# Kernel optimization log

Measured on AMD Instinct MI355X. Metric: run time of the kernel, lower is better.

## Reference

```python
import jax, jax.numpy as jnp
import numpy as np

B, P = 4, 2048
N = B * P
QD = 512            # query_dim == inner_dim (pos_emb is added to raw features)
CD = 512            # context_dim
HEADS, DH = 8, 64
INNER = HEADS * DH
SCALE = DH ** -0.5
HC, WC = 32, 32     # context spatial grid
L = HC * WC         # context_len
SELF_HW = 512       # spatial_dim[:2]
STRIDE = 8          # resolution_level == sparse tensor stride
PE_H = SELF_HW // STRIDE  # 64 BEV pos-emb grid


def setup_inputs() -> dict:
    key = jax.random.key(0)
    k = jax.random.split(key, 9)
    return {
        "feats": jax.random.normal(k[0], (N, QD), jnp.float32),
        "coords_xy": jax.random.randint(k[1], (N, 2), 0, SELF_HW),
        "context_emb": jax.random.normal(k[2], (B, HC, WC, CD), jnp.float32),
        "Wq": jax.random.normal(k[3], (QD, INNER), jnp.float32) * 0.02,
        "Wk": jax.random.normal(k[4], (CD, INNER), jnp.float32) * 0.02,
        "Wv": jax.random.normal(k[5], (CD, INNER), jnp.float32) * 0.02,
        "Wo": jax.random.normal(k[6], (INNER, QD), jnp.float32) * 0.02,
        "bo": jnp.zeros((QD,), jnp.float32),
        "pos_embedding": jax.random.normal(k[7], (PE_H, PE_H, INNER), jnp.float32) / INNER ** 0.5,
        "context_pos_embedding": jax.random.normal(k[8], (L, CD), jnp.float32) / INNER ** 0.5,
    }


def _neighbor_mask(coords_xy):
    # get_context_mask: scatter a (2*STRIDE+1)^2 neighborhood around each point's
    # projected context cell into a [N, L] boolean mask
    ratio = jnp.float32(HC) / jnp.float32(SELF_HW)
    center = jnp.round(coords_xy.astype(jnp.float32) * ratio).astype(jnp.int32)  # [N,2]
    off = jnp.stack(
        jnp.meshgrid(jnp.arange(-STRIDE, STRIDE + 1), jnp.arange(-STRIDE, STRIDE + 1), indexing="ij"),
        axis=-1,
    ).reshape(-1, 2)  # [K,2], K = 289
    pos = center[:, None, :] + off[None, :, :]        # [N,K,2]
    r = jnp.clip(pos[..., 0], 0, HC - 1)
    c = jnp.clip(pos[..., 1], 0, WC - 1)
    flat = r * WC + c                                  # [N,K]
    return jnp.zeros((N, L), jnp.bool_).at[jnp.arange(N)[:, None], flat].set(True)


def reference(feats, coords_xy, context_emb, Wq, Wk, Wv, Wo, bo, pos_embedding, context_pos_embedding):
    # get_context: add learned context positional embedding, flatten spatial -> [B, L, CD]
    ctx = (context_emb + context_pos_embedding.reshape(HC, WC, CD)).reshape(B, L, CD)
    # get_pos_emb: gather BEV positional embedding per point via floor(coord/stride)
    rc = coords_xy // STRIDE                           # [N,2] in [0, 64)
    pe = pos_embedding[rc[:, 0], rc[:, 1]]             # [N, INNER]
    f = (feats + pe).reshape(B, P, QD)                 # points grouped per batch (equal counts)
    mask = _neighbor_mask(coords_xy).reshape(B, P, L)
    q = (f @ Wq).reshape(B, P, HEADS, DH).transpose(0, 2, 1, 3)    # [B,h,P,d]
    k = (ctx @ Wk).reshape(B, L, HEADS, DH).transpose(0, 2, 1, 3)  # [B,h,L,d]
    v = (ctx @ Wv).reshape(B, L, HEADS, DH).transpose(0, 2, 1, 3)
    sim = jnp.einsum("bhid,bhjd->bhij", q, k) * SCALE              # [B,h,P,L]
    neg = -jnp.finfo(sim.dtype).max
    sim = jnp.where(mask[:, None, :, :], sim, neg)
    attn = jax.nn.softmax(sim, axis=-1)
    out = jnp.einsum("bhij,bhjd->bhid", attn, v)
    out = out.transpose(0, 2, 1, 3).reshape(B, P, INNER)
    out = out @ Wo + bo                                # to_out (dropout=0, eval)
    return out.reshape(N, QD)                          # scatter back to point features
```

## Files before the change

### kernel.cpp

```cpp
#include <hip/hip_runtime.h>


typedef __attribute__((ext_vector_type(8))) short bf16x8;
typedef __attribute__((ext_vector_type(4))) float f32x4;

#define SCL 0.18033688f

__device__ __forceinline__ unsigned short f2bf(float x) {
  union { float f; unsigned int u; } v; v.f = x;
  unsigned int r = v.u + 0x7FFFu + ((v.u >> 16) & 1u);
  return (unsigned short)(r >> 16);
}

__device__ __forceinline__ unsigned int pk2bf(float a, float b) {
  return (unsigned)f2bf(a) | ((unsigned)f2bf(b) << 16);
}

__device__ __forceinline__ unsigned int cvtpk(float a, float b) {
  unsigned int r;
  asm("v_cvt_pk_bf16_f32 %0, %1, %2" : "=v"(r) : "v"(a), "v"(b));
  return r;
}

__device__ __forceinline__ float fexp2(float x) {
#if __has_builtin(__builtin_amdgcn_exp2f)
  return __builtin_amdgcn_exp2f(x);
#else
  return exp2f(x);
#endif
}

__device__ __forceinline__ int swzb(int row, int chk) {
  return row * 128 + ((chk * 16) ^ ((row & 7) << 4));
}

__global__ __launch_bounds__(256) void prep_w(const float* __restrict__ Wq, const float* __restrict__ Wk,
                                              const float* __restrict__ Wv, const float* __restrict__ Wo,
                                              unsigned short* __restrict__ Wqt, unsigned short* __restrict__ Wkt,
                                              unsigned short* __restrict__ Wvt, unsigned short* __restrict__ Wot) {
  __shared__ float tile[64][65];
  const int bid = blockIdx.x;
  const int wsel = bid >> 6, tt = bid & 63;
  const int kt = (tt >> 3) << 6, ntb = (tt & 7) << 6;
  const float* W = (wsel == 0) ? Wq : (wsel == 1) ? Wk : (wsel == 2) ? Wv : Wo;
  unsigned short* Wt = (wsel == 0) ? Wqt : (wsel == 1) ? Wkt : (wsel == 2) ? Wvt : Wot;
  const int t = threadIdx.x;
#pragma unroll
  for (int p = 0; p < 16; ++p) {
    int e = p * 256 + t;
    int row = e >> 6, col = e & 63;
    tile[row][col] = W[(long)(kt + row) * 512 + ntb + col];
  }
  __syncthreads();
#pragma unroll
  for (int p = 0; p < 16; ++p) {
    int e = p * 256 + t;
    int n = e >> 6, k = e & 63;
    Wt[(long)(ntb + n) * 512 + kt + k] = f2bf(tile[k][n]);
  }
}

__global__ __launch_bounds__(256) void prep_in(const float* __restrict__ feats,
                                               const int* __restrict__ coords,
                                               const float* __restrict__ pos_emb,
                                               const float* __restrict__ ctx,
                                               const float* __restrict__ ctx_pos,
                                               unsigned short* __restrict__ Aq,
                                               unsigned short* __restrict__ Ac,
                                               int* __restrict__ perm) {
  if (blockIdx.x >= 6144) {
    __shared__ int hist[64];
    __shared__ int base[64];
    const int bb = blockIdx.x - 6144;
    const int t = threadIdx.x;
    if (t < 64) hist[t] = 0;
    __syncthreads();
    int keys[8];
#pragma unroll
    for (int i = 0; i < 8; ++i) {
      int q = bb * 2048 + t * 8 + i;
      int cr = (int)rintf((float)coords[2 * q] * 0.0625f);
      keys[i] = cr;
      atomicAdd(&hist[cr], 1);
    }
    __syncthreads();
    if (t == 0) {
      int s = 0;
      for (int k2 = 0; k2 < 64; ++k2) { base[k2] = s; s += hist[k2]; }
    }
    __syncthreads();
#pragma unroll
    for (int i = 0; i < 8; ++i) {
      int pos = atomicAdd(&base[keys[i]], 1);
      perm[bb * 2048 + pos] = t * 8 + i;
    }
    return;
  }
  int i = blockIdx.x * 256 + threadIdx.x;
  if (i < 1048576) {
    int e = i << 2;
    int q = e >> 9, k = e & 511;
    int pi = ((coords[2 * q] >> 3) << 6) + (coords[2 * q + 1] >> 3);
    float4 a = *(const float4*)(feats + e);
    float4 p = *(const float4*)(pos_emb + ((size_t)pi << 9) + k);
    uint2 o;
    o.x = pk2bf(a.x + p.x, a.y + p.y);
    o.y = pk2bf(a.z + p.z, a.w + p.w);
    *(uint2*)(Aq + e) = o;
  } else {
    int e = (i - 1048576) << 2;
    int r = e >> 9, k = e & 511;
    float4 a = *(const float4*)(ctx + e);
    float4 p = *(const float4*)(ctx_pos + ((size_t)(r & 1023) << 9) + k);
    uint2 o;
    o.x = pk2bf(a.x + p.x, a.y + p.y);
    o.y = pk2bf(a.z + p.z, a.w + p.w);
    *(uint2*)(Ac + e) = o;
  }
}

__global__ __launch_bounds__(256) void gemm_qkv(const unsigned short* __restrict__ Aq,
                                                const unsigned short* __restrict__ Ac,
                                                const unsigned short* __restrict__ Wqt,
                                                const unsigned short* __restrict__ Wkt,
                                                const unsigned short* __restrict__ Wvt,
                                                unsigned short* __restrict__ Qb,
                                                unsigned short* __restrict__ Kb,
                                                unsigned short* __restrict__ Vt) {
  __shared__ unsigned short As[128][72];
  __shared__ unsigned short Bs[128][72];
  const int t = threadIdx.x, l = t & 63, wid = t >> 6;
  const int wr = (wid >> 1) << 6, wc = (wid & 1) << 6;
  const int orig = blockIdx.x;
  const int bx = (orig & 7) * 64 + (orig >> 3);
  const bool isQ = bx < 256;
  long tm; const unsigned short* Bt; const unsigned short* Ab; bool isV = false; int nt;
  if (isQ) {
    tm = (long)(bx >> 2) * 128;
    nt = bx & 3;
    Bt = Wqt + (long)nt * 65536;
    Ab = Aq;
  } else {
    const int kvx = bx - 256;
    tm = (long)(kvx >> 3) * 128;
    const int y = kvx & 7;
    isV = y >= 4; nt = y & 3;
    Bt = (isV ? Wvt : Wkt) + (long)nt * 65536;
    Ab = Ac;
  }

  f32x4 acc[4][4] = {};
  const int lr = l & 15, lk = (l >> 4) << 3;
  const int srw = t >> 3, sch = (t & 7) << 3;

  for (int s = 0; s < 8; ++s) {
    const int k0 = s << 6;
    int4 rav[4], rbv[4];
#pragma unroll
    for (int p = 0; p < 4; ++p) {
      int row = srw + (p << 5);
      rav[p] = *(const int4*)(Ab + (tm + row) * 512 + k0 + sch);
      rbv[p] = *(const int4*)(Bt + (long)row * 512 + k0 + sch);
    }
#pragma unroll
    for (int p = 0; p < 4; ++p) {
      int row = srw + (p << 5);
      *(int4*)(&As[row][sch]) = rav[p];
      *(int4*)(&Bs[row][sch]) = rbv[p];
    }
    __syncthreads();
#pragma unroll
    for (int kk = 0; kk < 2; ++kk) {
      bf16x8 af[4], bfr[4];
#pragma unroll
      for (int i = 0; i < 4; ++i) af[i]  = *(const bf16x8*)(&As[wr + i * 16 + lr][kk * 32 + lk]);
#pragma unroll
      for (int i = 0; i < 4; ++i) bfr[i] = *(const bf16x8*)(&Bs[wc + i * 16 + lr][kk * 32 + lk]);
#pragma unroll
      for (int mi = 0; mi < 4; ++mi)
#pragma unroll
        for (int ni = 0; ni < 4; ++ni)
          acc[mi][ni] = __builtin_amdgcn_mfma_f32_16x16x32_bf16(af[mi], bfr[ni], acc[mi][ni], 0, 0, 0);
    }
    __syncthreads();
  }

  const int lq = (l >> 4) << 2;
#pragma unroll
  for (int mi = 0; mi < 4; ++mi)
#pragma unroll
    for (int ni = 0; ni < 4; ++ni) {
      int cn = nt * 128 + wc + ni * 16 + lr;
      long r0 = tm + wr + mi * 16 + lq;
      if (isQ) {
#pragma unroll
        for (int r = 0; r < 4; ++r)
          Qb[(r0 + r) * 512 + cn] = f2bf(acc[mi][ni][r] * SCL);
      } else if (!isV) {
#pragma unroll
        for (int r = 0; r < 4; ++r)
          Kb[(r0 + r) * 512 + cn] = f2bf(acc[mi][ni][r]);
      } else {
        int h = cn >> 6, d = cn & 63;
#pragma unroll
        for (int r = 0; r < 4; ++r) {
          long row = r0 + r;
          int b = (int)(row >> 10), j = (int)(row & 1023);
          int jp = (j & ~63) | ((j & 15) << 2) | ((j >> 4) & 3);
          Vt[((long)(b * 8 + h) * 64 + d) * 1024 + jp] = f2bf(acc[mi][ni][r]);
        }
      }
    }
}

__global__ __launch_bounds__(512, 4) void attn_mfma(const unsigned short* __restrict__ Qb,
                                                    const unsigned short* __restrict__ Kb,
                                                    const unsigned short* __restrict__ Vt,
                                                    const int* __restrict__ coords,
                                                    const int* __restrict__ perm,
                                                    unsigned short* __restrict__ Abf) {
  __shared__ char Kl[2][8192];
  __shared__ char Vl[2][8192];
  __shared__ char Ol[2048];
  __shared__ unsigned short Plds[8][16][72];
  __shared__ int permL[128];
  __shared__ int rng[2];
  const int t = threadIdx.x, w = t >> 6, l = t & 63;
  const int g = l >> 4, lc = l & 15;
  const int orig = blockIdx.x;
  const int sw = (orig & 7) * 64 + (orig >> 3);
  const int qx = sw & 15, bh = sw >> 4;
  const int b = bh >> 3, h = bh & 7;

  if (t < 128) permL[t] = perm[b * 2048 + qx * 128 + t];
  if (t == 0) { rng[0] = 63; rng[1] = 0; }
  __syncthreads();

  int rm[4], cm[4];
  int lrmin = 63, lrmax = 0;
#pragma unroll
  for (int r = 0; r < 4; ++r) {
    long qq = (long)b * 2048 + permL[w * 16 + g * 4 + r];
    int cr = (int)rintf((float)coords[2 * qq] * 0.0625f);
    int cc = (int)rintf((float)coords[2 * qq + 1] * 0.0625f);
    int rlo = max(0, cr - 8), rhi = min(31, cr + 8);
    int clo = max(0, cc - 8), chi = min(31, cc + 8);
    rm[r] = (int)((((unsigned)1 << (rhi - rlo + 1)) - 1) << rlo);
    cm[r] = (int)((((unsigned)1 << (chi - clo + 1)) - 1) << clo);
    lrmin = min(lrmin, rlo); lrmax = max(lrmax, rhi);
  }
#pragma unroll
  for (int off = 32; off > 0; off >>= 1) {
    lrmin = min(lrmin, __shfl_xor(lrmin, off));
    lrmax = max(lrmax, __shfl_xor(lrmax, off));
  }
  if (l == 0) { atomicMin(&rng[0], lrmin); atomicMax(&rng[1], lrmax); }

  bf16x8 qfr[2];
  {
    long qrow = (long)b * 2048 + permL[w * 16 + lc];
#pragma unroll
    for (int dc = 0; dc < 2; ++dc)
      qfr[dc] = *(const bf16x8*)(Qb + qrow * 512 + h * 64 + dc * 32 + g * 8);
  }

  const int srow = t >> 3, schk = t & 7;
  const unsigned short* Kg = Kb + ((long)b * 1024) * 512 + h * 64;
  const unsigned short* Vg = Vt + ((long)bh * 64) * 1024;

  if (t < 128) {
    int r = t >> 3, c = t & 7;
    unsigned short vv = (r == 0) ? (unsigned short)0x3F80 : (unsigned short)0;
    unsigned short tmp[8] = {vv, vv, vv, vv, vv, vv, vv, vv};
    *(int4*)(Ol + swzb(r, c)) = *(int4*)tmp;
  }
  __syncthreads();
  const int t0 = rng[0] >> 1, t1 = rng[1] >> 1;
  {
    const int kb0 = t0 * 64;
    int4 sk = *(const int4*)(Kg + (long)(kb0 + srow) * 512 + schk * 8);
    int4 sv_ = *(const int4*)(Vg + (long)srow * 1024 + kb0 + schk * 8);
    *(int4*)(Kl[0] + swzb(srow, schk)) = sk;
    *(int4*)(Vl[0] + swzb(srow, schk)) = sv_;
  }
  __syncthreads();

  f32x4 po[5] = {};

  for (int kt = t0; kt <= t1; ++kt) {
    const int cur = (kt - t0) & 1;
    const int kb = kt * 64;
    int4 nk = {}, nv = {};
    if (kt < t1) {
      const int kbn = kb + 64;
      nk = *(const int4*)(Kg + (long)(kbn + srow) * 512 + schk * 8);
      nv = *(const int4*)(Vg + (long)srow * 1024 + kbn + schk * 8);
    }

    bf16x8 kfr[4][2];
#pragma unroll
    for (int kf = 0; kf < 4; ++kf)
#pragma unroll
      for (int dc = 0; dc < 2; ++dc)
        kfr[kf][dc] = *(const bf16x8*)(Kl[cur] + swzb(kf * 16 + lc, dc * 4 + g));

    f32x4 sv[4];
#pragma unroll
    for (int kf = 0; kf < 4; ++kf) {
      f32x4 a = {};
      a = __builtin_amdgcn_mfma_f32_16x16x32_bf16(qfr[0], kfr[kf][0], a, 0, 0, 0);
      a = __builtin_amdgcn_mfma_f32_16x16x32_bf16(qfr[1], kfr[kf][1], a, 0, 0, 0);
      sv[kf] = a;
    }

    const int jrb = kb >> 5;
    int cmk[4][4];
#pragma unroll
    for (int kf = 0; kf < 4; ++kf) {
      int jr = jrb + (kf >> 1);
#pragma unroll
      for (int r = 0; r < 4; ++r)
        cmk[kf][r] = ((rm[r] >> jr) & 1) ? cm[r] : 0;
    }
#pragma unroll
    for (int kf = 0; kf < 4; ++kf) {
      int jc = ((kf & 1) << 4) + lc;
#pragma unroll
      for (int r = 0; r < 4; ++r) {
        float p = fexp2(sv[kf][r]);
        sv[kf][r] = ((cmk[kf][r] >> jc) & 1) ? p : 0.0f;
      }
    }

    bf16x8 vfr[5][2];
#pragma unroll
    for (int df = 0; df < 4; ++df)
#pragma unroll
      for (int kc = 0; kc < 2; ++kc)
        vfr[df][kc] = *(const bf16x8*)(Vl[cur] + swzb(df * 16 + lc, kc * 4 + g));
#pragma unroll
    for (int kc = 0; kc < 2; ++kc)
      vfr[4][kc] = *(const bf16x8*)(Ol + swzb(lc, kc * 4 + g));

#pragma unroll
    for (int r = 0; r < 4; ++r) {
      uint2 pk;
      pk.x = cvtpk(sv[0][r], sv[1][r]);
      pk.y = cvtpk(sv[2][r], sv[3][r]);
      *(uint2*)(&Plds[w][g * 4 + r][4 * lc]) = pk;
    }

    bf16x8 pa0 = *(const bf16x8*)(&Plds[w][lc][g * 8]);
    bf16x8 pa1 = *(const bf16x8*)(&Plds[w][lc][32 + g * 8]);
    __builtin_amdgcn_s_setprio(1);
#pragma unroll
    for (int df = 0; df < 5; ++df) {
      po[df] = __builtin_amdgcn_mfma_f32_16x16x32_bf16(pa0, vfr[df][0], po[df], 0, 0, 0);
      po[df] = __builtin_amdgcn_mfma_f32_16x16x32_bf16(pa1, vfr[df][1], po[df], 0, 0, 0);
    }
    __builtin_amdgcn_s_setprio(0);

    if (kt < t1) {
      const int nxt = cur ^ 1;
      *(int4*)(Kl[nxt] + swzb(srow, schk)) = nk;
      *(int4*)(Vl[nxt] + swzb(srow, schk)) = nv;
    }
    __syncthreads();
  }

#pragma unroll
  for (int r = 0; r < 4; ++r) {
    float lsum = __shfl(po[4][r], l & 48);
    float inv = 1.0f / lsum;
    long qr = (long)b * 2048 + permL[w * 16 + g * 4 + r];
#pragma unroll
    for (int df = 0; df < 4; ++df)
      Abf[qr * 512 + h * 64 + df * 16 + lc] = f2bf(po[df][r] * inv);
  }
}

__global__ __launch_bounds__(256) void gemm_o(const unsigned short* __restrict__ A,
                                              const unsigned short* __restrict__ Bt,
                                              float* __restrict__ C,
                                              const float* __restrict__ bias) {
  __shared__ unsigned short As[64][72];
  __shared__ unsigned short Bs[128][72];
  const int t = threadIdx.x, l = t & 63, wid = t >> 6;
  const int wr = (wid >> 1) << 5;
  const int wc = (wid & 1) << 6;
  const int orig = blockIdx.x;
  const int bx = (orig & 7) * 64 + (orig >> 3);
  const long tm = (long)(bx >> 2) * 64;
  const long tn = (long)(bx & 3) * 128;

  f32x4 acc[2][4] = {};
  const int lr = l & 15, lk = (l >> 4) << 3;
  for (int s = 0; s < 8; ++s) {
    const int k0 = s << 6;
    int4 rAv[2], rBv[4];
#pragma unroll
    for (int p = 0; p < 2; ++p) {
      int e = p * 256 + t;
      int row = e >> 3, ch = (e & 7) << 3;
      rAv[p] = *(const int4*)(A + (tm + row) * 512 + k0 + ch);
    }
#pragma unroll
    for (int p = 0; p < 4; ++p) {
      int e = p * 256 + t;
      int row = e >> 3, ch = (e & 7) << 3;
      rBv[p] = *(const int4*)(Bt + (tn + row) * 512 + k0 + ch);
    }
#pragma unroll
    for (int p = 0; p < 2; ++p) {
      int e = p * 256 + t;
      int row = e >> 3, ch = (e & 7) << 3;
      *(int4*)(&As[row][ch]) = rAv[p];
    }
#pragma unroll
    for (int p = 0; p < 4; ++p) {
      int e = p * 256 + t;
      int row = e >> 3, ch = (e & 7) << 3;
      *(int4*)(&Bs[row][ch]) = rBv[p];
    }
    __syncthreads();
#pragma unroll
    for (int kk = 0; kk < 2; ++kk) {
      bf16x8 af[2], bfr[4];
#pragma unroll
      for (int i = 0; i < 2; ++i) af[i]  = *(const bf16x8*)(&As[wr + i * 16 + lr][kk * 32 + lk]);
#pragma unroll
      for (int i = 0; i < 4; ++i) bfr[i] = *(const bf16x8*)(&Bs[wc + i * 16 + lr][kk * 32 + lk]);
#pragma unroll
      for (int mi = 0; mi < 2; ++mi)
#pragma unroll
        for (int ni = 0; ni < 4; ++ni)
          acc[mi][ni] = __builtin_amdgcn_mfma_f32_16x16x32_bf16(af[mi], bfr[ni], acc[mi][ni], 0, 0, 0);
    }
    __syncthreads();
  }

  const int lq = (l >> 4) << 2;
#pragma unroll
  for (int mi = 0; mi < 2; ++mi)
#pragma unroll
    for (int ni = 0; ni < 4; ++ni) {
      long col = tn + wc + ni * 16 + lr;
      float bv = bias[col];
      long r0 = tm + wr + mi * 16 + lq;
#pragma unroll
      for (int r = 0; r < 4; ++r)
        C[(r0 + r) * 512 + col] = acc[mi][ni][r] + bv;
    }
}

extern "C" void kernel_launch(void* const* d_in, const int* in_sizes, int n_in,
                              void* d_out, int out_size, void* d_ws, size_t ws_size,
                              hipStream_t stream) {
  (void)in_sizes; (void)n_in; (void)out_size; (void)ws_size;
  const float* feats   = (const float*)d_in[0];
  const int*   coords  = (const int*)d_in[1];
  const float* ctx     = (const float*)d_in[2];
  const float* Wq      = (const float*)d_in[3];
  const float* Wk      = (const float*)d_in[4];
  const float* Wv      = (const float*)d_in[5];
  const float* Wo      = (const float*)d_in[6];
  const float* bo      = (const float*)d_in[7];
  const float* pos_emb = (const float*)d_in[8];
  const float* ctx_pos = (const float*)d_in[9];
  float* out = (float*)d_out;
  char* ws = (char*)d_ws;

  unsigned short* Wqt = (unsigned short*)(ws);
  unsigned short* Wkt = (unsigned short*)(ws + 524288);
  unsigned short* Wvt = (unsigned short*)(ws + 1048576);
  unsigned short* Wot = (unsigned short*)(ws + 1572864);
  unsigned short* Aq  = (unsigned short*)(ws + 2097152);
  unsigned short* Ac  = (unsigned short*)(ws + 10485760);
  unsigned short* Qb  = (unsigned short*)(ws + 14680064);
  unsigned short* Kb  = (unsigned short*)(ws + 23068672);
  unsigned short* Vt  = (unsigned short*)(ws + 27262976);
  unsigned short* Abf = (unsigned short*)(ws + 31457280);
  int*            prm = (int*)(ws + 39845888);

  prep_w  <<<256, 256, 0, stream>>>(Wq, Wk, Wv, Wo, Wqt, Wkt, Wvt, Wot);
  prep_in <<<6148, 256, 0, stream>>>(feats, coords, pos_emb, ctx, ctx_pos, Aq, Ac, prm);
  gemm_qkv<<<512, 256, 0, stream>>>(Aq, Ac, Wqt, Wkt, Wvt, Qb, Kb, Vt);
  attn_mfma<<<512, 512, 0, stream>>>(Qb, Kb, Vt, coords, prm, Abf);
  gemm_o  <<<512, 256, 0, stream>>>(Abf, Wot, out, bo);
}
```

Baseline: 91.79 us.

## Double-buffer GEMM tiles via direct global-to-LDS loads; skip masked attention tiles per wave

```diff
diff --git a/kernel.cpp b/kernel.cpp
--- a/kernel.cpp
+++ b/kernel.cpp
@@ -28,6 +28,12 @@
 #else
   return exp2f(x);
 #endif
+}
+
+__device__ __forceinline__ void gload16(const unsigned short* g, char* l) {
+  __builtin_amdgcn_global_load_lds(
+      (const __attribute__((address_space(1))) unsigned int*)g,
+      (__attribute__((address_space(3))) unsigned int*)l, 16, 0, 0);
 }
 
 __device__ __forceinline__ int swzb(int row, int chk) {
@@ -127,10 +133,10 @@
                                                 unsigned short* __restrict__ Qb,
                                                 unsigned short* __restrict__ Kb,
                                                 unsigned short* __restrict__ Vt) {
-  __shared__ unsigned short As[128][72];
-  __shared__ unsigned short Bs[128][72];
-  const int t = threadIdx.x, l = t & 63, wid = t >> 6;
-  const int wr = (wid >> 1) << 6, wc = (wid & 1) << 6;
+  __shared__ char Asf[2][16384];
+  __shared__ char Bsf[2][16384];
+  const int t = threadIdx.x, l = t & 63, wv = t >> 6;
+  const int wr = (wv >> 1) << 6, wc = (wv & 1) << 6;
   const int orig = blockIdx.x;
   const int bx = (orig & 7) * 64 + (orig >> 3);
   const bool isQ = bx < 256;
@@ -149,33 +155,37 @@
     Ab = Ac;
   }
 
+  const int rr = l >> 3, chs = (l & 7) ^ rr;
+  auto STAGE = [&](int buf, int k0) {
+#pragma unroll
+    for (int i = 0; i < 4; ++i) {
+      int c = (wv << 2) + i;
+      int row = (c << 3) + rr;
+      gload16(Ab + (tm + row) * 512 + k0 + chs * 8, Asf[buf] + (c << 10));
+      gload16(Bt + (long)row * 512 + k0 + chs * 8, Bsf[buf] + (c << 10));
+    }
+  };
+
+  STAGE(0, 0);
+  __syncthreads();
+
   f32x4 acc[4][4] = {};
-  const int lr = l & 15, lk = (l >> 4) << 3;
-  const int srw = t >> 3, sch = (t & 7) << 3;
+  const int lr = l & 15, g = l >> 4;
 
   for (int s = 0; s < 8; ++s) {
-    const int k0 = s << 6;
-    int4 rav[4], rbv[4];
-#pragma unroll
-    for (int p = 0; p < 4; ++p) {
-      int row = srw + (p << 5);
-      rav[p] = *(const int4*)(Ab + (tm + row) * 512 + k0 + sch);
-      rbv[p] = *(const int4*)(Bt + (long)row * 512 + k0 + sch);
-    }
-#pragma unroll
-    for (int p = 0; p < 4; ++p) {
-      int row = srw + (p << 5);
-      *(int4*)(&As[row][sch]) = rav[p];
-      *(int4*)(&Bs[row][sch]) = rbv[p];
-    }
-    __syncthreads();
+    const int cur = s & 1;
+    if (s < 7) STAGE(cur ^ 1, (s + 1) << 6);
 #pragma unroll
     for (int kk = 0; kk < 2; ++kk) {
+      const int chd = (kk << 2) + g;
       bf16x8 af[4], bfr[4];
 #pragma unroll
-      for (int i = 0; i < 4; ++i) af[i]  = *(const bf16x8*)(&As[wr + i * 16 + lr][kk * 32 + lk]);
-#pragma unroll
-      for (int i = 0; i < 4; ++i) bfr[i] = *(const bf16x8*)(&Bs[wc + i * 16 + lr][kk * 32 + lk]);
+      for (int i = 0; i < 4; ++i) {
+        int ra = wr + i * 16 + lr;
+        int rb = wc + i * 16 + lr;
+        af[i]  = *(const bf16x8*)(Asf[cur] + swzb(ra, chd));
+        bfr[i] = *(const bf16x8*)(Bsf[cur] + swzb(rb, chd));
+      }
 #pragma unroll
       for (int mi = 0; mi < 4; ++mi)
 #pragma unroll
@@ -185,7 +195,7 @@
     __syncthreads();
   }
 
-  const int lq = (l >> 4) << 2;
+  const int lq = g << 2;
 #pragma unroll
   for (int mi = 0; mi < 4; ++mi)
 #pragma unroll
@@ -254,6 +264,7 @@
     lrmin = min(lrmin, __shfl_xor(lrmin, off));
     lrmax = max(lrmax, __shfl_xor(lrmax, off));
   }
+  const int wt0 = lrmin >> 1, wt1 = lrmax >> 1;
   if (l == 0) { atomicMin(&rng[0], lrmin); atomicMax(&rng[1], lrmax); }
 
   bf16x8 qfr[2];
@@ -297,68 +308,70 @@
       nv = *(const int4*)(Vg + (long)srow * 1024 + kbn + schk * 8);
     }
 
-    bf16x8 kfr[4][2];
-#pragma unroll
-    for (int kf = 0; kf < 4; ++kf)
-#pragma unroll
-      for (int dc = 0; dc < 2; ++dc)
-        kfr[kf][dc] = *(const bf16x8*)(Kl[cur] + swzb(kf * 16 + lc, dc * 4 + g));
-
-    f32x4 sv[4];
-#pragma unroll
-    for (int kf = 0; kf < 4; ++kf) {
-      f32x4 a = {};
-      a = __builtin_amdgcn_mfma_f32_16x16x32_bf16(qfr[0], kfr[kf][0], a, 0, 0, 0);
-      a = __builtin_amdgcn_mfma_f32_16x16x32_bf16(qfr[1], kfr[kf][1], a, 0, 0, 0);
-      sv[kf] = a;
-    }
-
-    const int jrb = kb >> 5;
-    int cmk[4][4];
-#pragma unroll
-    for (int kf = 0; kf < 4; ++kf) {
-      int jr = jrb + (kf >> 1);
-#pragma unroll
-      for (int r = 0; r < 4; ++r)
-        cmk[kf][r] = ((rm[r] >> jr) & 1) ? cm[r] : 0;
-    }
-#pragma unroll
-    for (int kf = 0; kf < 4; ++kf) {
-      int jc = ((kf & 1) << 4) + lc;
+    if (kt >= wt0 && kt <= wt1) {
+      bf16x8 kfr[4][2];
+#pragma unroll
+      for (int kf = 0; kf < 4; ++kf)
+#pragma unroll
+        for (int dc = 0; dc < 2; ++dc)
+          kfr[kf][dc] = *(const bf16x8*)(Kl[cur] + swzb(kf * 16 + lc, dc * 4 + g));
+
+      f32x4 sv[4];
+#pragma unroll
+      for (int kf = 0; kf < 4; ++kf) {
+        f32x4 a = {};
+        a = __builtin_amdgcn_mfma_f32_16x16x32_bf16(qfr[0], kfr[kf][0], a, 0, 0, 0);
+        a = __builtin_amdgcn_mfma_f32_16x16x32_bf16(qfr[1], kfr[kf][1], a, 0, 0, 0);
+        sv[kf] = a;
+      }
+
+      const int jrb = kb >> 5;
+      int cmk[4][4];
+#pragma unroll
+      for (int kf = 0; kf < 4; ++kf) {
+        int jr = jrb + (kf >> 1);
+#pragma unroll
+        for (int r = 0; r < 4; ++r)
+          cmk[kf][r] = ((rm[r] >> jr) & 1) ? cm[r] : 0;
+      }
+#pragma unroll
+      for (int kf = 0; kf < 4; ++kf) {
+        int jc = ((kf & 1) << 4) + lc;
+#pragma unroll
+        for (int r = 0; r < 4; ++r) {
+          float p = fexp2(sv[kf][r]);
+          sv[kf][r] = ((cmk[kf][r] >> jc) & 1) ? p : 0.0f;
+        }
+      }
+
+      bf16x8 vfr[5][2];
+#pragma unroll
+      for (int df = 0; df < 4; ++df)
+#pragma unroll
+        for (int kc = 0; kc < 2; ++kc)
+          vfr[df][kc] = *(const bf16x8*)(Vl[cur] + swzb(df * 16 + lc, kc * 4 + g));
+#pragma unroll
+      for (int kc = 0; kc < 2; ++kc)
+        vfr[4][kc] = *(const bf16x8*)(Ol + swzb(lc, kc * 4 + g));
+
 #pragma unroll
       for (int r = 0; r < 4; ++r) {
-        float p = fexp2(sv[kf][r]);
-        sv[kf][r] = ((cmk[kf][r] >> jc) & 1) ? p : 0.0f;
-      }
-    }
-
-    bf16x8 vfr[5][2];
-#pragma unroll
-    for (int df = 0; df < 4; ++df)
-#pragma unroll
-      for (int kc = 0; kc < 2; ++kc)
-        vfr[df][kc] = *(const bf16x8*)(Vl[cur] + swzb(df * 16 + lc, kc * 4 + g));
-#pragma unroll
-    for (int kc = 0; kc < 2; ++kc)
-      vfr[4][kc] = *(const bf16x8*)(Ol + swzb(lc, kc * 4 + g));
-
-#pragma unroll
-    for (int r = 0; r < 4; ++r) {
-      uint2 pk;
-      pk.x = cvtpk(sv[0][r], sv[1][r]);
-      pk.y = cvtpk(sv[2][r], sv[3][r]);
-      *(uint2*)(&Plds[w][g * 4 + r][4 * lc]) = pk;
-    }
-
-    bf16x8 pa0 = *(const bf16x8*)(&Plds[w][lc][g * 8]);
-    bf16x8 pa1 = *(const bf16x8*)(&Plds[w][lc][32 + g * 8]);
-    __builtin_amdgcn_s_setprio(1);
-#pragma unroll
-    for (int df = 0; df < 5; ++df) {
-      po[df] = __builtin_amdgcn_mfma_f32_16x16x32_bf16(pa0, vfr[df][0], po[df], 0, 0, 0);
-      po[df] = __builtin_amdgcn_mfma_f32_16x16x32_bf16(pa1, vfr[df][1], po[df], 0, 0, 0);
-    }
-    __builtin_amdgcn_s_setprio(0);
+        uint2 pk;
+        pk.x = cvtpk(sv[0][r], sv[1][r]);
+        pk.y = cvtpk(sv[2][r], sv[3][r]);
+        *(uint2*)(&Plds[w][g * 4 + r][4 * lc]) = pk;
+      }
+
+      bf16x8 pa0 = *(const bf16x8*)(&Plds[w][lc][g * 8]);
+      bf16x8 pa1 = *(const bf16x8*)(&Plds[w][lc][32 + g * 8]);
+      __builtin_amdgcn_s_setprio(1);
+#pragma unroll
+      for (int df = 0; df < 5; ++df) {
+        po[df] = __builtin_amdgcn_mfma_f32_16x16x32_bf16(pa0, vfr[df][0], po[df], 0, 0, 0);
+        po[df] = __builtin_amdgcn_mfma_f32_16x16x32_bf16(pa1, vfr[df][1], po[df], 0, 0, 0);
+      }
+      __builtin_amdgcn_s_setprio(0);
+    }
 
     if (kt < t1) {
       const int nxt = cur ^ 1;
@@ -383,53 +396,51 @@
                                               const unsigned short* __restrict__ Bt,
                                               float* __restrict__ C,
                                               const float* __restrict__ bias) {
-  __shared__ unsigned short As[64][72];
-  __shared__ unsigned short Bs[128][72];
-  const int t = threadIdx.x, l = t & 63, wid = t >> 6;
-  const int wr = (wid >> 1) << 5;
-  const int wc = (wid & 1) << 6;
+  __shared__ char Asf[2][8192];
+  __shared__ char Bsf[2][16384];
+  const int t = threadIdx.x, l = t & 63, wv = t >> 6;
+  const int wr = (wv >> 1) << 5;
+  const int wc = (wv & 1) << 6;
   const int orig = blockIdx.x;
   const int bx = (orig & 7) * 64 + (orig >> 3);
   const long tm = (long)(bx >> 2) * 64;
   const long tn = (long)(bx & 3) * 128;
 
+  const int rr = l >> 3, chs = (l & 7) ^ rr;
+  auto STAGE = [&](int buf, int k0) {
+#pragma unroll
+    for (int i = 0; i < 2; ++i) {
+      int c = (wv << 1) + i;
+      int row = (c << 3) + rr;
+      gload16(A + (tm + row) * 512 + k0 + chs * 8, Asf[buf] + (c << 10));
+    }
+#pragma unroll
+    for (int i = 0; i < 4; ++i) {
+      int c = (wv << 2) + i;
+      int row = (c << 3) + rr;
+      gload16(Bt + (tn + row) * 512 + k0 + chs * 8, Bsf[buf] + (c << 10));
+    }
+  };
+
+  STAGE(0, 0);
+  __syncthreads();
+
   f32x4 acc[2][4] = {};
-  const int lr = l & 15, lk = (l >> 4) << 3;
+  const int lr = l & 15, g = l >> 4;
+
   for (int s = 0; s < 8; ++s) {
-    const int k0 = s << 6;
-    int4 rAv[2], rBv[4];
-#pragma unroll
-    for (int p = 0; p < 2; ++p) {
-      int e = p * 256 + t;
-      int row = e >> 3, ch = (e & 7) << 3;
-      rAv[p] = *(const int4*)(A + (tm + row) * 512 + k0 + ch);
-    }
-#pragma unroll
-    for (int p = 0; p < 4; ++p) {
-      int e = p * 256 + t;
-      int row = e >> 3, ch = (e & 7) << 3;
-      rBv[p] = *(const int4*)(Bt + (tn + row) * 512 + k0 + ch);
-    }
-#pragma unroll
-    for (int p = 0; p < 2; ++p) {
-      int e = p * 256 + t;
-      int row = e >> 3, ch = (e & 7) << 3;
-      *(int4*)(&As[row][ch]) = rAv[p];
-    }
-#pragma unroll
-    for (int p = 0; p < 4; ++p) {
-      int e = p * 256 + t;
-      int row = e >> 3, ch = (e & 7) << 3;
-      *(int4*)(&Bs[row][ch]) = rBv[p];
-    }
-    __syncthreads();
+    const int cur = s & 1;
+    if (s < 7) STAGE(cur ^ 1, (s + 1) << 6);
 #pragma unroll
     for (int kk = 0; kk < 2; ++kk) {
+      const int chd = (kk << 2) + g;
       bf16x8 af[2], bfr[4];
 #pragma unroll
-      for (int i = 0; i < 2; ++i) af[i]  = *(const bf16x8*)(&As[wr + i * 16 + lr][kk * 32 + lk]);
-#pragma unroll
-      for (int i = 0; i < 4; ++i) bfr[i] = *(const bf16x8*)(&Bs[wc + i * 16 + lr][kk * 32 + lk]);
+      for (int i = 0; i < 2; ++i)
+        af[i] = *(const bf16x8*)(Asf[cur] + swzb(wr + i * 16 + lr, chd));
+#pragma unroll
+      for (int i = 0; i < 4; ++i)
+        bfr[i] = *(const bf16x8*)(Bsf[cur] + swzb(wc + i * 16 + lr, chd));
 #pragma unroll
       for (int mi = 0; mi < 2; ++mi)
 #pragma unroll
@@ -439,7 +450,7 @@
     __syncthreads();
   }
 
-  const int lq = (l >> 4) << 2;
+  const int lq = g << 2;
 #pragma unroll
   for (int mi = 0; mi < 2; ++mi)
 #pragma unroll
```

Measured after the change: 80.69 us. 1.14x faster.
